# Performance work log

Hardware: AMD Instinct MI355X
Metric: run time of the kernel (lower is better)

The kernel has to match this reference:

```python
import jax, jax.numpy as jnp
import numpy as np

K = 16  # hardcoded knn count in Density_loss.forward


def _knn_dist(x, k):
    """Squared pairwise distances [B,N,N], then k smallest per point -> [B,N,k]."""
    sq = jnp.sum(x * x, axis=-1)  # [B,N]
    # d[b,i,j] = |xi|^2 + |xj|^2 - 2 xi.xj
    d = sq[:, :, None] + sq[:, None, :] - 2.0 * jnp.einsum('bic,bjc->bij', x, x)
    neg_topk, _ = jax.lax.top_k(-d, k)  # k smallest distances
    return -neg_topk  # [B,N,k]


def setup_inputs() -> dict:
    key = jax.random.key(0)
    k1, k2 = jax.random.split(key)
    seed = jax.random.normal(k1, (8, 2048, 3), dtype=jnp.float32)
    gt_s = jax.random.normal(k2, (8, 2048, 3), dtype=jnp.float32)
    return {"seed": seed, "gt_s": gt_s}


def reference(seed, gt_s):
    seed_dis = _knn_dist(seed, K).mean(axis=-1)  # [B,N]
    gt_dis = _knn_dist(gt_s, K).mean(axis=-1)    # [B,N]
    # dis_avg=True branch: average over points -> [B], then MSE
    dis = seed_dis.mean(axis=-1)
    gt = gt_dis.mean(axis=-1)
    return jnp.mean((dis - gt) ** 2)
```

## Files before the change

### kernel.cpp

```cpp
#include <hip/hip_runtime.h>
#include <math.h>


#define NPTS 2048
#define KSEL 16
#define WAVES_PER_BLOCK 8
#define BLOCK (WAVES_PER_BLOCK * 64)
#define PTS_PER_BLOCK (WAVES_PER_BLOCK * 2)
#define NGROUPS (NPTS / PTS_PER_BLOCK)
#define NBLOCKS (2 * 8 * NGROUPS)

__device__ __forceinline__ int mbcnt64(unsigned long long m) {
  return __builtin_amdgcn_mbcnt_hi(
      (unsigned)(m >> 32), __builtin_amdgcn_mbcnt_lo((unsigned)m, 0u));
}

__device__ __forceinline__ float dist2(float px, float py, float pz,
                                       float cx, float cy, float cz) {
  float dx = px - cx, dy = py - cy, dz = pz - cz;
  return fmaf(dz, dz, fmaf(dy, dy, dx * dx));
}

__device__ __forceinline__ void gather_candidates(
    const float (&gm)[8], float thr, float px, float py, float pz, int lane,
    const float* xs, const float* ys, const float* zs, int* scrI, bool& ok,
    float& d0, float& d1, float& d2, float& d3) {
  unsigned qmask = 0u;
  int qg = 0;
  #pragma unroll
  for (int m = 0; m < 8; ++m) {
    const bool q = gm[m] <= thr;
    qmask |= q ? (1u << m) : 0u;
    qg += q ? 1 : 0;
  }
  const unsigned long long b0 = __ballot((qg & 1) != 0);
  const unsigned long long b1 = __ballot((qg & 2) != 0);
  const unsigned long long b2 = __ballot((qg & 4) != 0);
  const unsigned long long b3 = __ballot((qg & 8) != 0);
  const int pre =
      mbcnt64(b0) + 2 * mbcnt64(b1) + 4 * mbcnt64(b2) + 8 * mbcnt64(b3);
  const int tot = __popcll(b0) + 2 * __popcll(b1) + 4 * __popcll(b2) +
                  8 * __popcll(b3);
  ok = (tot <= 64);
  if (ok) {
    int pos = pre;
    #pragma unroll
    for (int m = 0; m < 8; ++m) {
      if ((qmask >> m) & 1u) {
        scrI[pos] = (lane << 3) | m;
        ++pos;
      }
    }
  }
  d0 = INFINITY; d1 = INFINITY; d2 = INFINITY; d3 = INFINITY;
  if (ok && lane < tot) {
    const int id = scrI[lane];
    const int o = ((id >> 3) << 2) + ((id & 7) << 8);
    const float4 cx4 = *(const float4*)&xs[o];
    const float4 cy4 = *(const float4*)&ys[o];
    const float4 cz4 = *(const float4*)&zs[o];
    d0 = dist2(px, py, pz, cx4.x, cy4.x, cz4.x);
    d1 = dist2(px, py, pz, cx4.y, cy4.y, cz4.y);
    d2 = dist2(px, py, pz, cx4.z, cy4.z, cz4.z);
    d3 = dist2(px, py, pz, cx4.w, cy4.w, cz4.w);
  }
}

__device__ float fallback_sum16(float px, float py, float pz, int lane,
                                const float* xs, const float* ys,
                                const float* zs) {
  float s = 0.f;
  unsigned consumed = 0u;
  #pragma unroll 1
  for (int r = 0; r < KSEL; ++r) {
    float bv = INFINITY;
    int bi = 0;
    #pragma unroll
    for (int m = 0; m < 8; ++m) {
      const int o = (lane << 2) + (m << 8);
      const float4 cx4 = *(const float4*)&xs[o];
      const float4 cy4 = *(const float4*)&ys[o];
      const float4 cz4 = *(const float4*)&zs[o];
      float dd;
      bool okb;
      dd = dist2(px, py, pz, cx4.x, cy4.x, cz4.x);
      okb = (((consumed >> ((m << 2) + 0)) & 1u) == 0u) && (dd < bv);
      bv = okb ? dd : bv; bi = okb ? ((m << 2) + 0) : bi;
      dd = dist2(px, py, pz, cx4.y, cy4.y, cz4.y);
      okb = (((consumed >> ((m << 2) + 1)) & 1u) == 0u) && (dd < bv);
      bv = okb ? dd : bv; bi = okb ? ((m << 2) + 1) : bi;
      dd = dist2(px, py, pz, cx4.z, cy4.z, cz4.z);
      okb = (((consumed >> ((m << 2) + 2)) & 1u) == 0u) && (dd < bv);
      bv = okb ? dd : bv; bi = okb ? ((m << 2) + 2) : bi;
      dd = dist2(px, py, pz, cx4.w, cy4.w, cz4.w);
      okb = (((consumed >> ((m << 2) + 3)) & 1u) == 0u) && (dd < bv);
      bv = okb ? dd : bv; bi = okb ? ((m << 2) + 3) : bi;
    }
    int bl = lane;
    #pragma unroll
    for (int ofs = 32; ofs >= 1; ofs >>= 1) {
      float ov = __shfl_xor(bv, ofs);
      int ol = __shfl_xor(bl, ofs);
      bool take = (ov < bv) || (ov == bv && ol < bl);
      bv = take ? ov : bv;
      bl = take ? ol : bl;
    }
    s += bv;
    if (lane == bl) consumed |= (1u << bi);
  }
  return s;
}

__global__ __launch_bounds__(BLOCK) void knn_sum16_kernel(
    const float* __restrict__ seed, const float* __restrict__ gt,
    float* __restrict__ out_part) {
  __shared__ float xs[NPTS];
  __shared__ float ys[NPTS];
  __shared__ float zs[NPTS];
  __shared__ int scrI[WAVES_PER_BLOCK][2][64];
  __shared__ float bsums[WAVES_PER_BLOCK];

  const int bid = blockIdx.x;
  const int t = bid >> 10;
  const int b = (bid >> 7) & 7;
  const int g = bid & 127;
  const float* base = (t == 0 ? seed : gt) + b * NPTS * 3;

  const int tid = threadIdx.x;

  {
    const float4* src = (const float4*)base;
    float4 f0 = src[3 * tid + 0];
    float4 f1 = src[3 * tid + 1];
    float4 f2 = src[3 * tid + 2];
    *(float4*)&xs[4 * tid] = make_float4(f0.x, f0.w, f1.z, f2.y);
    *(float4*)&ys[4 * tid] = make_float4(f0.y, f1.x, f1.w, f2.z);
    *(float4*)&zs[4 * tid] = make_float4(f0.z, f1.y, f2.x, f2.w);
  }
  __syncthreads();

  const int wave = tid >> 6;
  const int lane = tid & 63;
  const int iA = g * PTS_PER_BLOCK + wave * 2;
  const int iB = iA + 1;
  const float pax = xs[iA], pay = ys[iA], paz = zs[iA];
  const float pbx = xs[iB], pby = ys[iB], pbz = zs[iB];

  float gmA[8], gmB[8];
  #pragma unroll
  for (int m = 0; m < 8; ++m) {
    const int o = (lane << 2) + (m << 8);
    const float4 cx4 = *(const float4*)&xs[o];
    const float4 cy4 = *(const float4*)&ys[o];
    const float4 cz4 = *(const float4*)&zs[o];
    float a0 = dist2(pax, pay, paz, cx4.x, cy4.x, cz4.x);
    float a1 = dist2(pax, pay, paz, cx4.y, cy4.y, cz4.y);
    float a2 = dist2(pax, pay, paz, cx4.z, cy4.z, cz4.z);
    float a3 = dist2(pax, pay, paz, cx4.w, cy4.w, cz4.w);
    gmA[m] = fminf(fminf(a0, a1), fminf(a2, a3));
    float b0 = dist2(pbx, pby, pbz, cx4.x, cy4.x, cz4.x);
    float b1 = dist2(pbx, pby, pbz, cx4.y, cy4.y, cz4.y);
    float b2 = dist2(pbx, pby, pbz, cx4.z, cy4.z, cz4.z);
    float b3 = dist2(pbx, pby, pbz, cx4.w, cy4.w, cz4.w);
    gmB[m] = fminf(fminf(b0, b1), fminf(b2, b3));
  }
  float lminA = gmA[0], lminB = gmB[0];
  #pragma unroll
  for (int m = 1; m < 8; ++m) {
    lminA = fminf(lminA, gmA[m]);
    lminB = fminf(lminB, gmB[m]);
  }

  const unsigned uA = __float_as_uint(lminA);
  const unsigned uB = __float_as_uint(lminB);
  unsigned loA = 0u, hiA = 0x7F800000u, loB = 0u, hiB = 0x7F800000u;
  bool thA = false, thB = false;
  #pragma unroll 1
  for (int r = 0; r < 16; ++r) {
    if (thA && thB) break;
    const unsigned midA = (loA + hiA) >> 1;
    const unsigned midB = (loB + hiB) >> 1;
    const int cA = __popcll(__ballot(uA <= midA));
    const int cB = __popcll(__ballot(uB <= midB));
    if (!thA) {
      const bool gA = cA >= KSEL;
      hiA = gA ? midA : hiA;
      loA = gA ? loA : midA;
      thA = (cA >= KSEL) && (cA <= 24);
    }
    if (!thB) {
      const bool gB = cB >= KSEL;
      hiB = gB ? midB : hiB;
      loB = gB ? loB : midB;
      thB = (cB >= KSEL) && (cB <= 24);
    }
  }
  const float thrA = __uint_as_float(hiA);
  const float thrB = __uint_as_float(hiB);

  bool okA, okB;
  float a0, a1, a2, a3, b0, b1, b2, b3;
  gather_candidates(gmA, thrA, pax, pay, paz, lane, xs, ys, zs,
                    &scrI[wave][0][0], okA, a0, a1, a2, a3);
  gather_candidates(gmB, thrB, pbx, pby, pbz, lane, xs, ys, zs,
                    &scrI[wave][1][0], okB, b0, b1, b2, b3);

  const unsigned wa0 = __float_as_uint(a0) + 1u, wa1 = __float_as_uint(a1) + 1u;
  const unsigned wa2 = __float_as_uint(a2) + 1u, wa3 = __float_as_uint(a3) + 1u;
  const unsigned wb0 = __float_as_uint(b0) + 1u, wb1 = __float_as_uint(b1) + 1u;
  const unsigned wb2 = __float_as_uint(b2) + 1u, wb3 = __float_as_uint(b3) + 1u;
  unsigned eloA = 0u, ehiA = 0x7F800001u, eloB = 0u, ehiB = 0x7F800001u;
  bool hA = false, hB = false;
  unsigned sA = 0u, sB = 0u;
  #pragma unroll 1
  for (int r = 0; r < 32; ++r) {
    const bool needA = okA && !hA;
    const bool needB = okB && !hB;
    if (!(needA || needB)) break;
    const unsigned midA = (eloA + ehiA) >> 1;
    const unsigned midB = (eloB + ehiB) >> 1;
    const int cA = __popcll(__ballot(wa0 <= midA)) +
                   __popcll(__ballot(wa1 <= midA)) +
                   __popcll(__ballot(wa2 <= midA)) +
                   __popcll(__ballot(wa3 <= midA));
    const int cB = __popcll(__ballot(wb0 <= midB)) +
                   __popcll(__ballot(wb1 <= midB)) +
                   __popcll(__ballot(wb2 <= midB)) +
                   __popcll(__ballot(wb3 <= midB));
    if (needA) {
      if (cA >= KSEL) ehiA = midA; else eloA = midA;
      if (cA == KSEL) { hA = true; sA = midA; }
    }
    if (needB) {
      if (cB >= KSEL) ehiB = midB; else eloB = midB;
      if (cB == KSEL) { hB = true; sB = midB; }
    }
  }
  float extraA = 0.f, extraB = 0.f;
  if (okA && !hA) {
    sA = eloA;
    const int nlo = __popcll(__ballot(wa0 <= eloA)) +
                    __popcll(__ballot(wa1 <= eloA)) +
                    __popcll(__ballot(wa2 <= eloA)) +
                    __popcll(__ballot(wa3 <= eloA));
    extraA = (float)(KSEL - nlo) * __uint_as_float(ehiA - 1u);
  }
  if (okB && !hB) {
    sB = eloB;
    const int nlo = __popcll(__ballot(wb0 <= eloB)) +
                    __popcll(__ballot(wb1 <= eloB)) +
                    __popcll(__ballot(wb2 <= eloB)) +
                    __popcll(__ballot(wb3 <= eloB));
    extraB = (float)(KSEL - nlo) * __uint_as_float(ehiB - 1u);
  }
  float ca = 0.f, cb = 0.f;
  if (okA) {
    ca = ((wa0 <= sA) ? a0 : 0.f) + ((wa1 <= sA) ? a1 : 0.f) +
         ((wa2 <= sA) ? a2 : 0.f) + ((wa3 <= sA) ? a3 : 0.f);
  }
  if (okB) {
    cb = ((wb0 <= sB) ? b0 : 0.f) + ((wb1 <= sB) ? b1 : 0.f) +
         ((wb2 <= sB) ? b2 : 0.f) + ((wb3 <= sB) ? b3 : 0.f);
  }
  #pragma unroll
  for (int ofs = 32; ofs >= 1; ofs >>= 1) {
    ca += __shfl_xor(ca, ofs);
    cb += __shfl_xor(cb, ofs);
  }
  float sumA = ca + extraA;
  float sumB = cb + extraB;
  if (!okA) sumA = fallback_sum16(pax, pay, paz, lane, xs, ys, zs);
  if (!okB) sumB = fallback_sum16(pbx, pby, pbz, lane, xs, ys, zs);

  if (lane == 0) bsums[wave] = sumA + sumB;
  __syncthreads();
  if (tid == 0) {
    float s = 0.f;
    #pragma unroll
    for (int w = 0; w < WAVES_PER_BLOCK; ++w) s += bsums[w];
    out_part[bid] = s;
  }
}

__global__ __launch_bounds__(1024) void final_reduce_kernel(
    const float* __restrict__ parts, float* __restrict__ out) {
  __shared__ float partial[16];
  const int tid = threadIdx.x;
  const int wave = tid >> 6;
  const int lane = tid & 63;
  float s = parts[wave * NGROUPS + lane] + parts[wave * NGROUPS + 64 + lane];
  #pragma unroll
  for (int ofs = 32; ofs >= 1; ofs >>= 1) s += __shfl_xor(s, ofs);
  if (lane == 0) partial[wave] = s;
  __syncthreads();
  if (tid == 0) {
    const float scale = 1.f / (2048.f * 16.f);
    float acc = 0.f;
    #pragma unroll
    for (int bb = 0; bb < 8; ++bb) {
      float diff = (partial[bb] - partial[8 + bb]) * scale;
      acc += diff * diff;
    }
    out[0] = acc * 0.125f;
  }
}

extern "C" void kernel_launch(void* const* d_in, const int* in_sizes, int n_in,
                              void* d_out, int out_size, void* d_ws, size_t ws_size,
                              hipStream_t stream) {
  const float* seed = (const float*)d_in[0];
  const float* gt = (const float*)d_in[1];
  float* out = (float*)d_out;
  float* ws = (float*)d_ws;

  knn_sum16_kernel<<<NBLOCKS, BLOCK, 0, stream>>>(seed, gt, ws);
  final_reduce_kernel<<<1, 1024, 0, stream>>>(ws, out);
}
```

Measured before the change: 93.53 us.

## Process four query points per wave with packed half-precision group minima

Each wave now handles four query points instead of two, so each LDS float4 load of candidate coordinates is reused across more distance computations. This halves the block count and the per-block cost of staging the point cloud into shared memory. To keep register pressure down, the per-group minima are truncated to their upper 16 bits and packed two per register, and launch bounds now request occupancy. The truncated minima only decide which groups become candidates. Rounding down can over-admit a group and make the overflow fallback more likely, and four interleaved binary searches add serialized ballots per wave.

Result: slower. 100.9 us (+7.9%).

```diff
diff --git a/kernel.cpp b/kernel.cpp
--- a/kernel.cpp
+++ b/kernel.cpp
@@ -6,7 +6,8 @@
 #define KSEL 16
 #define WAVES_PER_BLOCK 8
 #define BLOCK (WAVES_PER_BLOCK * 64)
-#define PTS_PER_BLOCK (WAVES_PER_BLOCK * 2)
+#define QPW 4
+#define PTS_PER_BLOCK (WAVES_PER_BLOCK * QPW)
 #define NGROUPS (NPTS / PTS_PER_BLOCK)
 #define NBLOCKS (2 * 8 * NGROUPS)
 
@@ -22,17 +23,9 @@
 }
 
 __device__ __forceinline__ void gather_candidates(
-    const float (&gm)[8], float thr, float px, float py, float pz, int lane,
+    unsigned qmask, int qg, float px, float py, float pz, int lane,
     const float* xs, const float* ys, const float* zs, int* scrI, bool& ok,
     float& d0, float& d1, float& d2, float& d3) {
-  unsigned qmask = 0u;
-  int qg = 0;
-  #pragma unroll
-  for (int m = 0; m < 8; ++m) {
-    const bool q = gm[m] <= thr;
-    qmask |= q ? (1u << m) : 0u;
-    qg += q ? 1 : 0;
-  }
   const unsigned long long b0 = __ballot((qg & 1) != 0);
   const unsigned long long b1 = __ballot((qg & 2) != 0);
   const unsigned long long b2 = __ballot((qg & 4) != 0);
@@ -111,19 +104,19 @@
   return s;
 }
 
-__global__ __launch_bounds__(BLOCK) void knn_sum16_kernel(
+__global__ __launch_bounds__(BLOCK, 8) void knn_sum16_kernel(
     const float* __restrict__ seed, const float* __restrict__ gt,
     float* __restrict__ out_part) {
   __shared__ float xs[NPTS];
   __shared__ float ys[NPTS];
   __shared__ float zs[NPTS];
-  __shared__ int scrI[WAVES_PER_BLOCK][2][64];
+  __shared__ int scrI[WAVES_PER_BLOCK][QPW][64];
   __shared__ float bsums[WAVES_PER_BLOCK];
 
   const int bid = blockIdx.x;
-  const int t = bid >> 10;
-  const int b = (bid >> 7) & 7;
-  const int g = bid & 127;
+  const int t = bid >> 9;
+  const int b = (bid >> 6) & 7;
+  const int g = bid & 63;
   const float* base = (t == 0 ? seed : gt) + b * NPTS * 3;
 
   const int tid = threadIdx.x;
@@ -141,138 +134,153 @@
 
   const int wave = tid >> 6;
   const int lane = tid & 63;
-  const int iA = g * PTS_PER_BLOCK + wave * 2;
-  const int iB = iA + 1;
-  const float pax = xs[iA], pay = ys[iA], paz = zs[iA];
-  const float pbx = xs[iB], pby = ys[iB], pbz = zs[iB];
-
-  float gmA[8], gmB[8];
+  const int i0 = g * PTS_PER_BLOCK + wave * QPW;
+  float px[QPW], py[QPW], pz[QPW];
+  #pragma unroll
+  for (int qi = 0; qi < QPW; ++qi) {
+    px[qi] = xs[i0 + qi];
+    py[qi] = ys[i0 + qi];
+    pz[qi] = zs[i0 + qi];
+  }
+
+  unsigned pk[QPW][4];
+  float lmin[QPW] = {INFINITY, INFINITY, INFINITY, INFINITY};
+  float gprev[QPW];
   #pragma unroll
   for (int m = 0; m < 8; ++m) {
     const int o = (lane << 2) + (m << 8);
     const float4 cx4 = *(const float4*)&xs[o];
     const float4 cy4 = *(const float4*)&ys[o];
     const float4 cz4 = *(const float4*)&zs[o];
-    float a0 = dist2(pax, pay, paz, cx4.x, cy4.x, cz4.x);
-    float a1 = dist2(pax, pay, paz, cx4.y, cy4.y, cz4.y);
-    float a2 = dist2(pax, pay, paz, cx4.z, cy4.z, cz4.z);
-    float a3 = dist2(pax, pay, paz, cx4.w, cy4.w, cz4.w);
-    gmA[m] = fminf(fminf(a0, a1), fminf(a2, a3));
-    float b0 = dist2(pbx, pby, pbz, cx4.x, cy4.x, cz4.x);
-    float b1 = dist2(pbx, pby, pbz, cx4.y, cy4.y, cz4.y);
-    float b2 = dist2(pbx, pby, pbz, cx4.z, cy4.z, cz4.z);
-    float b3 = dist2(pbx, pby, pbz, cx4.w, cy4.w, cz4.w);
-    gmB[m] = fminf(fminf(b0, b1), fminf(b2, b3));
-  }
-  float lminA = gmA[0], lminB = gmB[0];
-  #pragma unroll
-  for (int m = 1; m < 8; ++m) {
-    lminA = fminf(lminA, gmA[m]);
-    lminB = fminf(lminB, gmB[m]);
-  }
-
-  const unsigned uA = __float_as_uint(lminA);
-  const unsigned uB = __float_as_uint(lminB);
-  unsigned loA = 0u, hiA = 0x7F800000u, loB = 0u, hiB = 0x7F800000u;
-  bool thA = false, thB = false;
+    #pragma unroll
+    for (int qi = 0; qi < QPW; ++qi) {
+      float d0 = dist2(px[qi], py[qi], pz[qi], cx4.x, cy4.x, cz4.x);
+      float d1 = dist2(px[qi], py[qi], pz[qi], cx4.y, cy4.y, cz4.y);
+      float d2 = dist2(px[qi], py[qi], pz[qi], cx4.z, cy4.z, cz4.z);
+      float d3 = dist2(px[qi], py[qi], pz[qi], cx4.w, cy4.w, cz4.w);
+      const float gm = fminf(fminf(d0, d1), fminf(d2, d3));
+      lmin[qi] = fminf(lmin[qi], gm);
+      if (m & 1) {
+        pk[qi][m >> 1] = (__float_as_uint(gprev[qi]) & 0xFFFF0000u) |
+                         (__float_as_uint(gm) >> 16);
+      } else {
+        gprev[qi] = gm;
+      }
+    }
+  }
+
+  unsigned ulm[QPW];
+  #pragma unroll
+  for (int qi = 0; qi < QPW; ++qi) ulm[qi] = __float_as_uint(lmin[qi]);
+  unsigned lo4[QPW] = {0u, 0u, 0u, 0u};
+  unsigned hi4[QPW] = {0x7F800000u, 0x7F800000u, 0x7F800000u, 0x7F800000u};
+  bool done[QPW] = {false, false, false, false};
   #pragma unroll 1
   for (int r = 0; r < 16; ++r) {
-    if (thA && thB) break;
-    const unsigned midA = (loA + hiA) >> 1;
-    const unsigned midB = (loB + hiB) >> 1;
-    const int cA = __popcll(__ballot(uA <= midA));
-    const int cB = __popcll(__ballot(uB <= midB));
-    if (!thA) {
-      const bool gA = cA >= KSEL;
-      hiA = gA ? midA : hiA;
-      loA = gA ? loA : midA;
-      thA = (cA >= KSEL) && (cA <= 24);
-    }
-    if (!thB) {
-      const bool gB = cB >= KSEL;
-      hiB = gB ? midB : hiB;
-      loB = gB ? loB : midB;
-      thB = (cB >= KSEL) && (cB <= 24);
-    }
-  }
-  const float thrA = __uint_as_float(hiA);
-  const float thrB = __uint_as_float(hiB);
-
-  bool okA, okB;
-  float a0, a1, a2, a3, b0, b1, b2, b3;
-  gather_candidates(gmA, thrA, pax, pay, paz, lane, xs, ys, zs,
-                    &scrI[wave][0][0], okA, a0, a1, a2, a3);
-  gather_candidates(gmB, thrB, pbx, pby, pbz, lane, xs, ys, zs,
-                    &scrI[wave][1][0], okB, b0, b1, b2, b3);
-
-  const unsigned wa0 = __float_as_uint(a0) + 1u, wa1 = __float_as_uint(a1) + 1u;
-  const unsigned wa2 = __float_as_uint(a2) + 1u, wa3 = __float_as_uint(a3) + 1u;
-  const unsigned wb0 = __float_as_uint(b0) + 1u, wb1 = __float_as_uint(b1) + 1u;
-  const unsigned wb2 = __float_as_uint(b2) + 1u, wb3 = __float_as_uint(b3) + 1u;
-  unsigned eloA = 0u, ehiA = 0x7F800001u, eloB = 0u, ehiB = 0x7F800001u;
-  bool hA = false, hB = false;
-  unsigned sA = 0u, sB = 0u;
+    if (done[0] && done[1] && done[2] && done[3]) break;
+    #pragma unroll
+    for (int qi = 0; qi < QPW; ++qi) {
+      if (!done[qi]) {
+        const unsigned mid = (lo4[qi] + hi4[qi]) >> 1;
+        const int c = __popcll(__ballot(ulm[qi] <= mid));
+        const bool ge = c >= KSEL;
+        hi4[qi] = ge ? mid : hi4[qi];
+        lo4[qi] = ge ? lo4[qi] : mid;
+        done[qi] = ge && (c <= 24);
+      }
+    }
+  }
+
+  unsigned qmask[QPW];
+  int qg[QPW];
+  #pragma unroll
+  for (int qi = 0; qi < QPW; ++qi) {
+    const float thr = __uint_as_float(hi4[qi]);
+    unsigned qm = 0u;
+    int c = 0;
+    #pragma unroll
+    for (int mm = 0; mm < 4; ++mm) {
+      const float ge = __uint_as_float(pk[qi][mm] & 0xFFFF0000u);
+      const float go = __uint_as_float(pk[qi][mm] << 16);
+      if (ge <= thr) { qm |= 1u << (2 * mm); ++c; }
+      if (go <= thr) { qm |= 1u << (2 * mm + 1); ++c; }
+    }
+    qmask[qi] = qm;
+    qg[qi] = c;
+  }
+
+  bool okq[QPW];
+  unsigned wq[QPW][4];
+  #pragma unroll
+  for (int qi = 0; qi < QPW; ++qi) {
+    float d0, d1, d2, d3;
+    gather_candidates(qmask[qi], qg[qi], px[qi], py[qi], pz[qi], lane, xs, ys,
+                      zs, &scrI[wave][qi][0], okq[qi], d0, d1, d2, d3);
+    wq[qi][0] = __float_as_uint(d0) + 1u;
+    wq[qi][1] = __float_as_uint(d1) + 1u;
+    wq[qi][2] = __float_as_uint(d2) + 1u;
+    wq[qi][3] = __float_as_uint(d3) + 1u;
+  }
+
+  unsigned elo[QPW] = {0u, 0u, 0u, 0u};
+  unsigned ehi[QPW] = {0x7F800001u, 0x7F800001u, 0x7F800001u, 0x7F800001u};
+  bool h[QPW] = {false, false, false, false};
+  unsigned sel[QPW] = {0u, 0u, 0u, 0u};
   #pragma unroll 1
   for (int r = 0; r < 32; ++r) {
-    const bool needA = okA && !hA;
-    const bool needB = okB && !hB;
-    if (!(needA || needB)) break;
-    const unsigned midA = (eloA + ehiA) >> 1;
-    const unsigned midB = (eloB + ehiB) >> 1;
-    const int cA = __popcll(__ballot(wa0 <= midA)) +
-                   __popcll(__ballot(wa1 <= midA)) +
-                   __popcll(__ballot(wa2 <= midA)) +
-                   __popcll(__ballot(wa3 <= midA));
-    const int cB = __popcll(__ballot(wb0 <= midB)) +
-                   __popcll(__ballot(wb1 <= midB)) +
-                   __popcll(__ballot(wb2 <= midB)) +
-                   __popcll(__ballot(wb3 <= midB));
-    if (needA) {
-      if (cA >= KSEL) ehiA = midA; else eloA = midA;
-      if (cA == KSEL) { hA = true; sA = midA; }
-    }
-    if (needB) {
-      if (cB >= KSEL) ehiB = midB; else eloB = midB;
-      if (cB == KSEL) { hB = true; sB = midB; }
-    }
-  }
-  float extraA = 0.f, extraB = 0.f;
-  if (okA && !hA) {
-    sA = eloA;
-    const int nlo = __popcll(__ballot(wa0 <= eloA)) +
-                    __popcll(__ballot(wa1 <= eloA)) +
-                    __popcll(__ballot(wa2 <= eloA)) +
-                    __popcll(__ballot(wa3 <= eloA));
-    extraA = (float)(KSEL - nlo) * __uint_as_float(ehiA - 1u);
-  }
-  if (okB && !hB) {
-    sB = eloB;
-    const int nlo = __popcll(__ballot(wb0 <= eloB)) +
-                    __popcll(__ballot(wb1 <= eloB)) +
-                    __popcll(__ballot(wb2 <= eloB)) +
-                    __popcll(__ballot(wb3 <= eloB));
-    extraB = (float)(KSEL - nlo) * __uint_as_float(ehiB - 1u);
-  }
-  float ca = 0.f, cb = 0.f;
-  if (okA) {
-    ca = ((wa0 <= sA) ? a0 : 0.f) + ((wa1 <= sA) ? a1 : 0.f) +
-         ((wa2 <= sA) ? a2 : 0.f) + ((wa3 <= sA) ? a3 : 0.f);
-  }
-  if (okB) {
-    cb = ((wb0 <= sB) ? b0 : 0.f) + ((wb1 <= sB) ? b1 : 0.f) +
-         ((wb2 <= sB) ? b2 : 0.f) + ((wb3 <= sB) ? b3 : 0.f);
+    bool any = false;
+    #pragma unroll
+    for (int qi = 0; qi < QPW; ++qi) any = any || (okq[qi] && !h[qi]);
+    if (!any) break;
+    #pragma unroll
+    for (int qi = 0; qi < QPW; ++qi) {
+      if (okq[qi] && !h[qi]) {
+        const unsigned mid = (elo[qi] + ehi[qi]) >> 1;
+        const int c = __popcll(__ballot(wq[qi][0] <= mid)) +
+                      __popcll(__ballot(wq[qi][1] <= mid)) +
+                      __popcll(__ballot(wq[qi][2] <= mid)) +
+                      __popcll(__ballot(wq[qi][3] <= mid));
+        if (c >= KSEL) ehi[qi] = mid; else elo[qi] = mid;
+        if (c == KSEL) { h[qi] = true; sel[qi] = mid; }
+      }
+    }
+  }
+  float extra[QPW];
+  float cs[QPW];
+  #pragma unroll
+  for (int qi = 0; qi < QPW; ++qi) {
+    extra[qi] = 0.f;
+    if (okq[qi] && !h[qi]) {
+      sel[qi] = elo[qi];
+      const int nlo = __popcll(__ballot(wq[qi][0] <= elo[qi])) +
+                      __popcll(__ballot(wq[qi][1] <= elo[qi])) +
+                      __popcll(__ballot(wq[qi][2] <= elo[qi])) +
+                      __popcll(__ballot(wq[qi][3] <= elo[qi]));
+      extra[qi] = (float)(KSEL - nlo) * __uint_as_float(ehi[qi] - 1u);
+    }
+    float c = 0.f;
+    if (okq[qi]) {
+      #pragma unroll
+      for (int j = 0; j < 4; ++j) {
+        c += (wq[qi][j] <= sel[qi]) ? __uint_as_float(wq[qi][j] - 1u) : 0.f;
+      }
+    }
+    cs[qi] = c;
   }
   #pragma unroll
   for (int ofs = 32; ofs >= 1; ofs >>= 1) {
-    ca += __shfl_xor(ca, ofs);
-    cb += __shfl_xor(cb, ofs);
-  }
-  float sumA = ca + extraA;
-  float sumB = cb + extraB;
-  if (!okA) sumA = fallback_sum16(pax, pay, paz, lane, xs, ys, zs);
-  if (!okB) sumB = fallback_sum16(pbx, pby, pbz, lane, xs, ys, zs);
-
-  if (lane == 0) bsums[wave] = sumA + sumB;
+    #pragma unroll
+    for (int qi = 0; qi < QPW; ++qi) cs[qi] += __shfl_xor(cs[qi], ofs);
+  }
+  float wsum = 0.f;
+  #pragma unroll
+  for (int qi = 0; qi < QPW; ++qi) {
+    float s = cs[qi] + extra[qi];
+    if (!okq[qi]) s = fallback_sum16(px[qi], py[qi], pz[qi], lane, xs, ys, zs);
+    wsum += s;
+  }
+
+  if (lane == 0) bsums[wave] = wsum;
   __syncthreads();
   if (tid == 0) {
     float s = 0.f;
@@ -288,7 +296,7 @@
   const int tid = threadIdx.x;
   const int wave = tid >> 6;
   const int lane = tid & 63;
-  float s = parts[wave * NGROUPS + lane] + parts[wave * NGROUPS + 64 + lane];
+  float s = parts[wave * NGROUPS + lane];
   #pragma unroll
   for (int ofs = 32; ofs >= 1; ofs >>= 1) s += __shfl_xor(s, ofs);
   if (lane == 0) partial[wave] = s;
```
